# Optimization experiments

Hardware: AMD Instinct MI355X
Metric: run time of the kernel (lower is better)

The kernel has to match this reference:

```python
import jax, jax.numpy as jnp
import numpy as np

B, C, K = 8192, 4096, 4096
BK, BN = 1, 16          # block-sparse tile sizes (bk x bn)
KEEP = 0.3


def setup_inputs() -> dict:
    key = jax.random.key(0)
    kx, kw, kb, km = jax.random.split(key, 4)
    stdv = 1.0 / np.sqrt(C * K)  # reset_parameters uses 1/sqrt(C*K)
    x = jax.random.normal(kx, (B, C), dtype=jnp.float32)
    weight = jax.random.uniform(kw, (K, C), dtype=jnp.float32, minval=-stdv, maxval=stdv)
    # block mask on (K/bk, C/bn) grid, expanded to full weight shape
    blk = (jax.random.uniform(km, (K // BK, C // BN)) < KEEP).astype(jnp.float32)
    mask = jnp.repeat(jnp.repeat(blk, BK, axis=0), BN, axis=1)  # [K, C]
    weight = weight * mask
    bias = jax.random.uniform(kb, (K,), dtype=jnp.float32, minval=-stdv, maxval=stdv)
    return {"x": x, "weight": weight, "bias": bias}


def reference(x, weight, bias):
    # SparseLinearRelu forward (sparse-kernel path, attr='relu'):
    # y = relu(x @ W^T + b); zero blocks of W contribute nothing (skipped by kernel).
    return jax.nn.relu(jnp.dot(x, weight.T) + bias)
```

## Files before the change

kernel.cpp:

```cpp
#include <hip/hip_runtime.h>
#include <hip/hip_bf16.h>

typedef __attribute__((ext_vector_type(4))) float f32x4;
typedef __attribute__((ext_vector_type(8))) short bf16x8;
typedef __attribute__((ext_vector_type(4))) short bf16x4v;

#define M_DIM 8192
#define N_DIM 4096
#define K_DIM 4096
#define NX (M_DIM * K_DIM)
#define NW (N_DIM * K_DIM)

#define BM 256
#define BN 256
#define BK 32
#define NKT (K_DIM / BK)
#define THREADS 512

#define GLOAD_LDS16(g, l)                                                        \
  __builtin_amdgcn_global_load_lds(                                              \
      (const __attribute__((address_space(1))) void*)(g),                        \
      (__attribute__((address_space(3))) void*)(l), 16, 0, 0)

__global__ __launch_bounds__(256) void convert_bf16(const float* __restrict__ x,
                                                    const float* __restrict__ w,
                                                    short* __restrict__ ws) {
  const long stride = (long)gridDim.x * blockDim.x;
  const long total8 = ((long)NX + NW) / 8;
  for (long i = blockIdx.x * (long)blockDim.x + threadIdx.x; i < total8; i += stride) {
    const long base = i * 8;
    const float* src;
    short* dst;
    if (base < NX) {
      src = x + base;
      dst = ws + base;
    } else {
      src = w + (base - NX);
      dst = ws + base;
    }
    f32x4 a = *(const f32x4*)src;
    f32x4 b = *(const f32x4*)(src + 4);
    bf16x8 o;
    o[0] = (short)__bfloat16_as_ushort(__float2bfloat16(a[0]));
    o[1] = (short)__bfloat16_as_ushort(__float2bfloat16(a[1]));
    o[2] = (short)__bfloat16_as_ushort(__float2bfloat16(a[2]));
    o[3] = (short)__bfloat16_as_ushort(__float2bfloat16(a[3]));
    o[4] = (short)__bfloat16_as_ushort(__float2bfloat16(b[0]));
    o[5] = (short)__bfloat16_as_ushort(__float2bfloat16(b[1]));
    o[6] = (short)__bfloat16_as_ushort(__float2bfloat16(b[2]));
    o[7] = (short)__bfloat16_as_ushort(__float2bfloat16(b[3]));
    *(bf16x8*)dst = o;
  }
}

__global__ __launch_bounds__(THREADS, 2) void gemm256_bf16(
    const short* __restrict__ Abf,
    const short* __restrict__ Bbf,
    const float* __restrict__ bias,
    float* __restrict__ Y) {
  __shared__ short lds[3 * 16384];

  const int tid  = threadIdx.x;
  const int lane = tid & 63;
  const int wave = tid >> 6;
  const int wm   = wave >> 2;
  const int wn   = wave & 3;

  const long rowA0 = (long)blockIdx.y * BM;
  const long rowB0 = (long)blockIdx.x * BN;

  const int s_row_lo = wave * 16 + (lane >> 2);
  const int s_phys   = lane & 3;

  f32x4 acc[8][4];
#pragma unroll
  for (int i = 0; i < 8; ++i)
#pragma unroll
    for (int j = 0; j < 4; ++j) acc[i][j] = (f32x4)0.0f;

  auto stage = [&](int buf, int kt) {
#pragma unroll
    for (int is = 0; is < 2; ++is) {
      const int row     = is * 128 + s_row_lo;
      const int logical = s_phys ^ ((row >> 1) & 3);
      const long gcol   = (long)kt * BK + logical * 8;
      GLOAD_LDS16(Abf + (rowA0 + row) * (long)K_DIM + gcol,
                  &lds[buf * 16384 + is * 4096 + wave * 512]);
      GLOAD_LDS16(Bbf + (rowB0 + row) * (long)K_DIM + gcol,
                  &lds[buf * 16384 + 8192 + is * 4096 + wave * 512]);
    }
  };

  const int frow = lane & 15;
  const int fsl  = lane >> 4;

  stage(0, 0);
  stage(1, 1);
  asm volatile("s_waitcnt vmcnt(4)" ::: "memory");
  __builtin_amdgcn_s_barrier();
  __builtin_amdgcn_sched_barrier(0);

  for (int kt = 0; kt < NKT; ++kt) {
    const int cur = kt % 3;
    if (kt + 2 < NKT) stage((kt + 2) % 3, kt + 2);

    const short* As = &lds[cur * 16384];
    const short* Bs = &lds[cur * 16384 + 8192];
    bf16x8 af[8], bfr[4];
#pragma unroll
    for (int i = 0; i < 8; ++i) {
      const int row = wm * 128 + i * 16 + frow;
      const int ph  = fsl ^ ((row >> 1) & 3);
      af[i] = *(const bf16x8*)&As[row * 32 + ph * 8];
    }
#pragma unroll
    for (int j = 0; j < 4; ++j) {
      const int row = wn * 64 + j * 16 + frow;
      const int ph  = fsl ^ ((row >> 1) & 3);
      bfr[j] = *(const bf16x8*)&Bs[row * 32 + ph * 8];
    }

    __builtin_amdgcn_s_setprio(1);
#pragma unroll
    for (int i = 0; i < 8; ++i)
#pragma unroll
      for (int j = 0; j < 4; ++j)
        acc[i][j] = __builtin_amdgcn_mfma_f32_16x16x32_bf16(af[i], bfr[j], acc[i][j], 0, 0, 0);
    __builtin_amdgcn_s_setprio(0);

    if (kt + 1 < NKT) {
      if (kt + 2 < NKT)
        asm volatile("s_waitcnt vmcnt(4)" ::: "memory");
      else
        asm volatile("s_waitcnt vmcnt(0)" ::: "memory");
      __builtin_amdgcn_s_barrier();
      __builtin_amdgcn_sched_barrier(0);
    }
  }

  const int c0 = lane & 15;
  const int r0 = (lane >> 4) * 4;
#pragma unroll
  for (int j = 0; j < 4; ++j) {
    const long gc = rowB0 + wn * 64 + j * 16 + c0;
    const float bv = bias[gc];
#pragma unroll
    for (int i = 0; i < 8; ++i) {
      const long gr0 = rowA0 + wm * 128 + i * 16 + r0;
#pragma unroll
      for (int r = 0; r < 4; ++r) {
        float v = acc[i][j][r] + bv;
        Y[(gr0 + r) * (long)N_DIM + gc] = fmaxf(v, 0.0f);
      }
    }
  }
}

#define FBM 128
#define FBK 32
#define FLDSS 40
__global__ __launch_bounds__(256) void fallback_gemm(
    const float* __restrict__ X, const float* __restrict__ W,
    const float* __restrict__ bias, float* __restrict__ Y) {
  __shared__ short As[FBM * FLDSS];
  __shared__ short Bs[FBM * FLDSS];
  const int tid = threadIdx.x, lane = tid & 63, wave = tid >> 6;
  const int wm = (wave >> 1) * 64, wn = (wave & 1) * 64;
  const long rowA0 = (long)blockIdx.y * FBM, rowB0 = (long)blockIdx.x * FBM;
  const int srow = tid >> 3, scol = (tid & 7) * 4;
  const float* Aptr = X + (rowA0 + srow) * (long)K_DIM + scol;
  const float* Bptr = W + (rowB0 + srow) * (long)K_DIM + scol;
  f32x4 ra[4], rb[4];
#pragma unroll
  for (int i = 0; i < 4; ++i) {
    ra[i] = *(const f32x4*)(Aptr + (long)i * 32 * K_DIM);
    rb[i] = *(const f32x4*)(Bptr + (long)i * 32 * K_DIM);
  }
  f32x4 acc[4][4];
#pragma unroll
  for (int i = 0; i < 4; ++i)
#pragma unroll
    for (int j = 0; j < 4; ++j) acc[i][j] = (f32x4)0.0f;
  for (int kt = 0; kt < K_DIM / FBK; ++kt) {
    __syncthreads();
#pragma unroll
    for (int i = 0; i < 4; ++i) {
      bf16x4v pa, pb;
#pragma unroll
      for (int j = 0; j < 4; ++j) {
        pa[j] = (short)__bfloat16_as_ushort(__float2bfloat16(ra[i][j]));
        pb[j] = (short)__bfloat16_as_ushort(__float2bfloat16(rb[i][j]));
      }
      *(bf16x4v*)&As[(i * 32 + srow) * FLDSS + scol] = pa;
      *(bf16x4v*)&Bs[(i * 32 + srow) * FLDSS + scol] = pb;
    }
    if (kt + 1 < K_DIM / FBK) {
      const float* An = Aptr + (kt + 1) * FBK;
      const float* Bn = Bptr + (kt + 1) * FBK;
#pragma unroll
      for (int i = 0; i < 4; ++i) {
        ra[i] = *(const f32x4*)(An + (long)i * 32 * K_DIM);
        rb[i] = *(const f32x4*)(Bn + (long)i * 32 * K_DIM);
      }
    }
    __syncthreads();
    bf16x8 af[4], bfr[4];
#pragma unroll
    for (int i = 0; i < 4; ++i) {
      af[i]  = *(const bf16x8*)&As[(wm + i * 16 + (lane & 15)) * FLDSS + (lane >> 4) * 8];
      bfr[i] = *(const bf16x8*)&Bs[(wn + i * 16 + (lane & 15)) * FLDSS + (lane >> 4) * 8];
    }
#pragma unroll
    for (int i = 0; i < 4; ++i)
#pragma unroll
      for (int j = 0; j < 4; ++j)
        acc[i][j] = __builtin_amdgcn_mfma_f32_16x16x32_bf16(af[i], bfr[j], acc[i][j], 0, 0, 0);
  }
  const int r0 = (lane >> 4) * 4, c0 = lane & 15;
#pragma unroll
  for (int j = 0; j < 4; ++j) {
    const long gc = rowB0 + wn + j * 16 + c0;
    const float bv = bias[gc];
#pragma unroll
    for (int i = 0; i < 4; ++i) {
      const long gr0 = rowA0 + wm + i * 16 + r0;
#pragma unroll
      for (int r = 0; r < 4; ++r) {
        float v = acc[i][j][r] + bv;
        Y[(gr0 + r) * (long)N_DIM + gc] = fmaxf(v, 0.0f);
      }
    }
  }
}

extern "C" void kernel_launch(void* const* d_in, const int* in_sizes, int n_in,
                              void* d_out, int out_size, void* d_ws, size_t ws_size,
                              hipStream_t stream) {
  const float* x = (const float*)d_in[0];
  const float* w = (const float*)d_in[1];
  const float* b = (const float*)d_in[2];
  float* y = (float*)d_out;

  const size_t need = (size_t)(NX + NW) * sizeof(short);
  if (ws_size >= need) {
    short* ws = (short*)d_ws;
    convert_bf16<<<2048, 256, 0, stream>>>(x, w, ws);
    dim3 grid(N_DIM / BN, M_DIM / BM);
    gemm256_bf16<<<grid, dim3(THREADS), 0, stream>>>(ws, ws + NX, b, y);
  } else {
    dim3 grid(N_DIM / FBM, M_DIM / FBM);
    fallback_gemm<<<grid, dim3(256), 0, stream>>>(x, w, b, y);
  }
}
```

Measured before the change: 291.8 us.

## Restructure GEMM main loop into 4-phase ping-pong with BK=64 staged loads

```diff
diff --git a/kernel.cpp b/kernel.cpp
--- a/kernel.cpp
+++ b/kernel.cpp
@@ -13,7 +13,7 @@
 
 #define BM 256
 #define BN 256
-#define BK 32
+#define BK 64
 #define NKT (K_DIM / BK)
 #define THREADS 512
 
@@ -29,15 +29,8 @@
   const long total8 = ((long)NX + NW) / 8;
   for (long i = blockIdx.x * (long)blockDim.x + threadIdx.x; i < total8; i += stride) {
     const long base = i * 8;
-    const float* src;
-    short* dst;
-    if (base < NX) {
-      src = x + base;
-      dst = ws + base;
-    } else {
-      src = w + (base - NX);
-      dst = ws + base;
-    }
+    const float* src = (base < NX) ? (x + base) : (w + (base - NX));
+    short* dst = ws + base;
     f32x4 a = *(const f32x4*)src;
     f32x4 b = *(const f32x4*)(src + 4);
     bf16x8 o;
@@ -58,7 +51,8 @@
     const short* __restrict__ Bbf,
     const float* __restrict__ bias,
     float* __restrict__ Y) {
-  __shared__ short lds[3 * 16384];
+  __shared__ short lds[2 * 32768];
+  char* const ldsb = (char*)lds;
 
   const int tid  = threadIdx.x;
   const int lane = tid & 63;
@@ -69,8 +63,19 @@
   const long rowA0 = (long)blockIdx.y * BM;
   const long rowB0 = (long)blockIdx.x * BN;
 
-  const int s_row_lo = wave * 16 + (lane >> 2);
-  const int s_phys   = lane & 3;
+  const int sg_col = (((lane & 7) ^ ((lane >> 3) & 7)) << 3);
+  const int s_rlo  = wave * 8 + (lane >> 3);
+
+  const int offk0 = (lane & 15) * 128 + ((((lane >> 4)) ^ (lane & 7)) << 4);
+  const int offk1 = (lane & 15) * 128 + (((4 + (lane >> 4)) ^ (lane & 7)) << 4);
+
+  auto stage = [&](char* bufb, int half, int tt) {
+    const long grow = (half < 2 ? rowA0 + (long)half * 128 : rowB0 + (long)(half - 2) * 128) + s_rlo;
+    const short* g = (half < 2 ? Abf : Bbf) + grow * (long)K_DIM + (long)tt * BK + sg_col;
+    char* l = bufb + half * 16384 + wave * 1024;
+    GLOAD_LDS16(g, l);
+    GLOAD_LDS16(g + 64 * (long)K_DIM, l + 8192);
+  };
 
   f32x4 acc[8][4];
 #pragma unroll
@@ -78,64 +83,107 @@
 #pragma unroll
     for (int j = 0; j < 4; ++j) acc[i][j] = (f32x4)0.0f;
 
-  auto stage = [&](int buf, int kt) {
-#pragma unroll
-    for (int is = 0; is < 2; ++is) {
-      const int row     = is * 128 + s_row_lo;
-      const int logical = s_phys ^ ((row >> 1) & 3);
-      const long gcol   = (long)kt * BK + logical * 8;
-      GLOAD_LDS16(Abf + (rowA0 + row) * (long)K_DIM + gcol,
-                  &lds[buf * 16384 + is * 4096 + wave * 512]);
-      GLOAD_LDS16(Bbf + (rowB0 + row) * (long)K_DIM + gcol,
-                  &lds[buf * 16384 + 8192 + is * 4096 + wave * 512]);
-    }
-  };
-
-  const int frow = lane & 15;
-  const int fsl  = lane >> 4;
-
-  stage(0, 0);
-  stage(1, 1);
+  stage(ldsb, 0, 0);
+  stage(ldsb, 1, 0);
+  stage(ldsb, 2, 0);
+  stage(ldsb, 3, 0);
+  stage(ldsb + 65536, 0, 1);
+  stage(ldsb + 65536, 2, 1);
   asm volatile("s_waitcnt vmcnt(4)" ::: "memory");
   __builtin_amdgcn_s_barrier();
-  __builtin_amdgcn_sched_barrier(0);
-
-  for (int kt = 0; kt < NKT; ++kt) {
-    const int cur = kt % 3;
-    if (kt + 2 < NKT) stage((kt + 2) % 3, kt + 2);
-
-    const short* As = &lds[cur * 16384];
-    const short* Bs = &lds[cur * 16384 + 8192];
-    bf16x8 af[8], bfr[4];
-#pragma unroll
-    for (int i = 0; i < 8; ++i) {
-      const int row = wm * 128 + i * 16 + frow;
-      const int ph  = fsl ^ ((row >> 1) & 3);
-      af[i] = *(const bf16x8*)&As[row * 32 + ph * 8];
-    }
-#pragma unroll
-    for (int j = 0; j < 4; ++j) {
-      const int row = wn * 64 + j * 16 + frow;
-      const int ph  = fsl ^ ((row >> 1) & 3);
-      bfr[j] = *(const bf16x8*)&Bs[row * 32 + ph * 8];
-    }
-
+
+  bf16x8 af[4][2], bfr[4][2];
+
+  for (int t = 0; t < NKT; ++t) {
+    const int c = t & 1;
+    const char* ldsA = ldsb + c * 65536 + wm * 16384;
+    const char* ldsB = ldsb + c * 65536 + 32768 + (wn >> 1) * 16384 + (wn & 1) * 8192;
+    char* bnx  = ldsb + (c ^ 1) * 65536;
+    char* bnx2 = ldsb + c * 65536;
+
+#pragma unroll
+    for (int m = 0; m < 4; ++m) {
+      af[m][0] = *(const bf16x8*)(ldsA + m * 2048 + offk0);
+      af[m][1] = *(const bf16x8*)(ldsA + m * 2048 + offk1);
+    }
+#pragma unroll
+    for (int n = 0; n < 2; ++n) {
+      bfr[n][0] = *(const bf16x8*)(ldsB + n * 2048 + offk0);
+      bfr[n][1] = *(const bf16x8*)(ldsB + n * 2048 + offk1);
+    }
+    if (t + 1 < NKT) stage(bnx, 1, t + 1);
+    asm volatile("s_waitcnt lgkmcnt(8)" ::: "memory");
+    __builtin_amdgcn_s_barrier();
+    asm volatile("s_waitcnt lgkmcnt(0)" ::: "memory");
+    __builtin_amdgcn_sched_barrier(0);
     __builtin_amdgcn_s_setprio(1);
 #pragma unroll
-    for (int i = 0; i < 8; ++i)
-#pragma unroll
-      for (int j = 0; j < 4; ++j)
-        acc[i][j] = __builtin_amdgcn_mfma_f32_16x16x32_bf16(af[i], bfr[j], acc[i][j], 0, 0, 0);
+    for (int kk = 0; kk < 2; ++kk)
+#pragma unroll
+      for (int m = 0; m < 4; ++m)
+#pragma unroll
+        for (int n = 0; n < 2; ++n)
+          acc[m][n] = __builtin_amdgcn_mfma_f32_16x16x32_bf16(af[m][kk], bfr[n][kk], acc[m][n], 0, 0, 0);
     __builtin_amdgcn_s_setprio(0);
-
-    if (kt + 1 < NKT) {
-      if (kt + 2 < NKT)
-        asm volatile("s_waitcnt vmcnt(4)" ::: "memory");
-      else
-        asm volatile("s_waitcnt vmcnt(0)" ::: "memory");
-      __builtin_amdgcn_s_barrier();
-      __builtin_amdgcn_sched_barrier(0);
-    }
+    __builtin_amdgcn_s_barrier();
+
+#pragma unroll
+    for (int n = 2; n < 4; ++n) {
+      bfr[n][0] = *(const bf16x8*)(ldsB + n * 2048 + offk0);
+      bfr[n][1] = *(const bf16x8*)(ldsB + n * 2048 + offk1);
+    }
+    if (t + 1 < NKT) stage(bnx, 3, t + 1);
+    __builtin_amdgcn_s_barrier();
+    asm volatile("s_waitcnt lgkmcnt(0)" ::: "memory");
+    __builtin_amdgcn_sched_barrier(0);
+    __builtin_amdgcn_s_setprio(1);
+#pragma unroll
+    for (int kk = 0; kk < 2; ++kk)
+#pragma unroll
+      for (int m = 0; m < 4; ++m)
+#pragma unroll
+        for (int n = 2; n < 4; ++n)
+          acc[m][n] = __builtin_amdgcn_mfma_f32_16x16x32_bf16(af[m][kk], bfr[n][kk], acc[m][n], 0, 0, 0);
+    __builtin_amdgcn_s_setprio(0);
+    __builtin_amdgcn_s_barrier();
+
+#pragma unroll
+    for (int m = 0; m < 4; ++m) {
+      af[m][0] = *(const bf16x8*)(ldsA + (4 + m) * 2048 + offk0);
+      af[m][1] = *(const bf16x8*)(ldsA + (4 + m) * 2048 + offk1);
+    }
+    __builtin_amdgcn_s_barrier();
+    asm volatile("s_waitcnt lgkmcnt(0)" ::: "memory");
+    __builtin_amdgcn_sched_barrier(0);
+    __builtin_amdgcn_s_setprio(1);
+#pragma unroll
+    for (int kk = 0; kk < 2; ++kk)
+#pragma unroll
+      for (int m = 0; m < 4; ++m)
+#pragma unroll
+        for (int n = 0; n < 2; ++n)
+          acc[4 + m][n] = __builtin_amdgcn_mfma_f32_16x16x32_bf16(af[m][kk], bfr[n][kk], acc[4 + m][n], 0, 0, 0);
+    __builtin_amdgcn_s_setprio(0);
+    __builtin_amdgcn_s_barrier();
+
+    if (t + 2 < NKT) {
+      stage(bnx2, 0, t + 2);
+      stage(bnx2, 2, t + 2);
+    }
+    __builtin_amdgcn_s_setprio(1);
+#pragma unroll
+    for (int kk = 0; kk < 2; ++kk)
+#pragma unroll
+      for (int m = 0; m < 4; ++m)
+#pragma unroll
+        for (int n = 2; n < 4; ++n)
+          acc[4 + m][n] = __builtin_amdgcn_mfma_f32_16x16x32_bf16(af[m][kk], bfr[n][kk], acc[4 + m][n], 0, 0, 0);
+    __builtin_amdgcn_s_setprio(0);
+    if (t + 2 < NKT)
+      asm volatile("s_waitcnt vmcnt(4)" ::: "memory");
+    else
+      asm volatile("s_waitcnt vmcnt(0)" ::: "memory");
+    __builtin_amdgcn_s_barrier();
   }
 
   const int c0 = lane & 15;
```

New measurement: 281.7 us. -3.5%, faster.

## Restructure bf16 GEMM main loop into double-buffered BK=64 ping-pong schedule

Applied to the files above, without the earlier changes.

```diff
diff --git a/kernel.cpp b/kernel.cpp
--- a/kernel.cpp
+++ b/kernel.cpp
@@ -13,7 +13,7 @@
 
 #define BM 256
 #define BN 256
-#define BK 32
+#define BK 64
 #define NKT (K_DIM / BK)
 #define THREADS 512
 
@@ -29,15 +29,8 @@
   const long total8 = ((long)NX + NW) / 8;
   for (long i = blockIdx.x * (long)blockDim.x + threadIdx.x; i < total8; i += stride) {
     const long base = i * 8;
-    const float* src;
-    short* dst;
-    if (base < NX) {
-      src = x + base;
-      dst = ws + base;
-    } else {
-      src = w + (base - NX);
-      dst = ws + base;
-    }
+    const float* src = (base < NX) ? (x + base) : (w + (base - NX));
+    short* dst = ws + base;
     f32x4 a = *(const f32x4*)src;
     f32x4 b = *(const f32x4*)(src + 4);
     bf16x8 o;
@@ -58,7 +51,8 @@
     const short* __restrict__ Bbf,
     const float* __restrict__ bias,
     float* __restrict__ Y) {
-  __shared__ short lds[3 * 16384];
+  __shared__ short lds[2 * 32768];
+  char* const ldsb = (char*)lds;
 
   const int tid  = threadIdx.x;
   const int lane = tid & 63;
@@ -66,11 +60,105 @@
   const int wm   = wave >> 2;
   const int wn   = wave & 3;
 
-  const long rowA0 = (long)blockIdx.y * BM;
-  const long rowB0 = (long)blockIdx.x * BN;
-
-  const int s_row_lo = wave * 16 + (lane >> 2);
-  const int s_phys   = lane & 3;
+  const int lin = blockIdx.x + blockIdx.y * (N_DIM / BN);
+  const int swz = (lin & 7) * 64 + (lin >> 3);
+  const int bx = swz & 15;
+  const int by = swz >> 4;
+  const long rowA0 = (long)by * BM;
+  const long rowB0 = (long)bx * BN;
+
+  const int sg_col = (((lane & 7) ^ ((lane >> 3) & 7)) << 3);
+  const int s_row  = wave * 8 + (lane >> 3);
+
+  const short* gA = Abf + (rowA0 + s_row) * (long)K_DIM + sg_col;
+  const short* gB = Bbf + (rowB0 + s_row) * (long)K_DIM + sg_col;
+
+  const int offk0 = (lane & 15) * 128 + ((((lane >> 4)) ^ (lane & 7)) << 4);
+  const int offk1 = (lane & 15) * 128 + (((4 + (lane >> 4)) ^ (lane & 7)) << 4);
+
+#define STAGE_A(BOFF_, TT) do {                                                  \
+    const short* g_ = gA + (long)(TT) * BK;                                      \
+    _Pragma("unroll")                                                            \
+    for (int is_ = 0; is_ < 4; ++is_)                                            \
+      GLOAD_LDS16(g_ + (long)is_ * 64 * K_DIM,                                   \
+                  ldsb + (BOFF_) + is_ * 8192 + wave * 1024);                    \
+  } while (0)
+
+#define STAGE_B(BOFF_, TT) do {                                                  \
+    const short* g_ = gB + (long)(TT) * BK;                                      \
+    _Pragma("unroll")                                                            \
+    for (int is_ = 0; is_ < 4; ++is_)                                            \
+      GLOAD_LDS16(g_ + (long)is_ * 64 * K_DIM,                                   \
+                  ldsb + (BOFF_) + 32768 + is_ * 8192 + wave * 1024);            \
+  } while (0)
+
+#define PH_READ_A(DST, BOFF_, MADD) do {                                         \
+    const char* pa_ = ldsb + (BOFF_) + wm * 16384 + (MADD);                      \
+    _Pragma("unroll")                                                            \
+    for (int m_ = 0; m_ < 4; ++m_) {                                             \
+      DST[m_][0] = *(const bf16x8*)(pa_ + m_ * 2048 + offk0);                    \
+      DST[m_][1] = *(const bf16x8*)(pa_ + m_ * 2048 + offk1);                    \
+    }                                                                            \
+  } while (0)
+
+#define PH_READ_B(DST, BOFF_, NADD) do {                                         \
+    const char* pb_ = ldsb + (BOFF_) + 32768 + wn * 8192 + (NADD);               \
+    _Pragma("unroll")                                                            \
+    for (int n_ = 0; n_ < 2; ++n_) {                                             \
+      DST[n_][0] = *(const bf16x8*)(pb_ + n_ * 2048 + offk0);                    \
+      DST[n_][1] = *(const bf16x8*)(pb_ + n_ * 2048 + offk1);                    \
+    }                                                                            \
+  } while (0)
+
+#define MFMA16(AF, BF, MB, NB) do {                                              \
+    __builtin_amdgcn_s_setprio(1);                                               \
+    _Pragma("unroll")                                                            \
+    for (int kk_ = 0; kk_ < 2; ++kk_)                                            \
+      _Pragma("unroll")                                                          \
+      for (int m_ = 0; m_ < 4; ++m_)                                             \
+        _Pragma("unroll")                                                        \
+        for (int n_ = 0; n_ < 2; ++n_)                                           \
+          acc[(MB) + m_][(NB) + n_] = __builtin_amdgcn_mfma_f32_16x16x32_bf16(   \
+              AF[m_][kk_], BF[n_][kk_], acc[(MB) + m_][(NB) + n_], 0, 0, 0);     \
+    __builtin_amdgcn_s_setprio(0);                                               \
+  } while (0)
+
+#define TILE(CUR, ALT, BOFF_, NOFF_, T, DO_ST, DO_PF, VM8) do {                  \
+                              \
+    asm volatile("s_waitcnt lgkmcnt(0)" ::: "memory");                           \
+    __builtin_amdgcn_sched_barrier(0);                                           \
+    PH_READ_A(ALT, BOFF_, 8192);                                                 \
+    __builtin_amdgcn_sched_barrier(0);                                           \
+    MFMA16(CUR, bfr01, 0, 0);                                                    \
+    __builtin_amdgcn_s_barrier();                                                \
+                               \
+    asm volatile("s_waitcnt lgkmcnt(0)" ::: "memory");                           \
+    __builtin_amdgcn_sched_barrier(0);                                           \
+    PH_READ_B(bfr23, BOFF_, 4096);                                               \
+    __builtin_amdgcn_sched_barrier(0);                                           \
+    MFMA16(ALT, bfr01, 4, 0);                                                    \
+    __builtin_amdgcn_s_barrier();                                                \
+                                  \
+    asm volatile("s_waitcnt lgkmcnt(0)" ::: "memory");                           \
+    __builtin_amdgcn_sched_barrier(0);                                           \
+    if (DO_ST) STAGE_A(BOFF_, (T) + 2);                                          \
+    __builtin_amdgcn_sched_barrier(0);                                           \
+    MFMA16(ALT, bfr23, 4, 2);                                                    \
+    __builtin_amdgcn_s_barrier();                                                \
+         \
+                 \
+    if (DO_ST) STAGE_B(BOFF_, (T) + 2);                                          \
+    if (DO_PF) {                                                                 \
+      if (VM8) asm volatile("s_waitcnt vmcnt(8)" ::: "memory");                  \
+      else     asm volatile("s_waitcnt vmcnt(0)" ::: "memory");                  \
+      __builtin_amdgcn_s_barrier();                                              \
+      __builtin_amdgcn_sched_barrier(0);                                         \
+      PH_READ_A(ALT, NOFF_, 0);                                                  \
+      PH_READ_B(bfr01, NOFF_, 0);                                                \
+      __builtin_amdgcn_sched_barrier(0);                                         \
+    }                                                                            \
+    MFMA16(CUR, bfr23, 0, 2);                                                    \
+  } while (0)
 
   f32x4 acc[8][4];
 #pragma unroll
@@ -78,65 +166,33 @@
 #pragma unroll
     for (int j = 0; j < 4; ++j) acc[i][j] = (f32x4)0.0f;
 
-  auto stage = [&](int buf, int kt) {
-#pragma unroll
-    for (int is = 0; is < 2; ++is) {
-      const int row     = is * 128 + s_row_lo;
-      const int logical = s_phys ^ ((row >> 1) & 3);
-      const long gcol   = (long)kt * BK + logical * 8;
-      GLOAD_LDS16(Abf + (rowA0 + row) * (long)K_DIM + gcol,
-                  &lds[buf * 16384 + is * 4096 + wave * 512]);
-      GLOAD_LDS16(Bbf + (rowB0 + row) * (long)K_DIM + gcol,
-                  &lds[buf * 16384 + 8192 + is * 4096 + wave * 512]);
-    }
-  };
-
-  const int frow = lane & 15;
-  const int fsl  = lane >> 4;
-
-  stage(0, 0);
-  stage(1, 1);
-  asm volatile("s_waitcnt vmcnt(4)" ::: "memory");
+  bf16x8 afA[4][2], afB[4][2], bfr01[2][2], bfr23[2][2];
+
+  STAGE_A(0, 0);
+  STAGE_B(0, 0);
+  STAGE_A(65536, 1);
+  STAGE_B(65536, 1);
+  asm volatile("s_waitcnt vmcnt(8)" ::: "memory");
   __builtin_amdgcn_s_barrier();
   __builtin_amdgcn_sched_barrier(0);
-
-  for (int kt = 0; kt < NKT; ++kt) {
-    const int cur = kt % 3;
-    if (kt + 2 < NKT) stage((kt + 2) % 3, kt + 2);
-
-    const short* As = &lds[cur * 16384];
-    const short* Bs = &lds[cur * 16384 + 8192];
-    bf16x8 af[8], bfr[4];
-#pragma unroll
-    for (int i = 0; i < 8; ++i) {
-      const int row = wm * 128 + i * 16 + frow;
-      const int ph  = fsl ^ ((row >> 1) & 3);
-      af[i] = *(const bf16x8*)&As[row * 32 + ph * 8];
-    }
-#pragma unroll
-    for (int j = 0; j < 4; ++j) {
-      const int row = wn * 64 + j * 16 + frow;
-      const int ph  = fsl ^ ((row >> 1) & 3);
-      bfr[j] = *(const bf16x8*)&Bs[row * 32 + ph * 8];
-    }
-
-    __builtin_amdgcn_s_setprio(1);
-#pragma unroll
-    for (int i = 0; i < 8; ++i)
-#pragma unroll
-      for (int j = 0; j < 4; ++j)
-        acc[i][j] = __builtin_amdgcn_mfma_f32_16x16x32_bf16(af[i], bfr[j], acc[i][j], 0, 0, 0);
-    __builtin_amdgcn_s_setprio(0);
-
-    if (kt + 1 < NKT) {
-      if (kt + 2 < NKT)
-        asm volatile("s_waitcnt vmcnt(4)" ::: "memory");
-      else
-        asm volatile("s_waitcnt vmcnt(0)" ::: "memory");
-      __builtin_amdgcn_s_barrier();
-      __builtin_amdgcn_sched_barrier(0);
-    }
-  }
+  PH_READ_A(afA, 0, 0);
+  PH_READ_B(bfr01, 0, 0);
+  __builtin_amdgcn_sched_barrier(0);
+
+  for (int tp = 0; tp < NKT / 2 - 1; ++tp) {
+    const int t0 = 2 * tp;
+    TILE(afA, afB, 0, 65536, t0, 1, 1, 1);
+    TILE(afB, afA, 65536, 0, t0 + 1, 1, 1, 1);
+  }
+  TILE(afA, afB, 0, 65536, NKT - 2, 0, 1, 0);
+  TILE(afB, afA, 65536, 0, NKT - 1, 0, 0, 0);
+
+#undef TILE
+#undef MFMA16
+#undef PH_READ_B
+#undef PH_READ_A
+#undef STAGE_B
+#undef STAGE_A
 
   const int c0 = lane & 15;
   const int r0 = (lane >> 4) * 4;
```

Measured after the change: 281.8 us. 1.04x faster.
